# Optimization experiments

Hardware: AMD Instinct MI355X
Metric: run time of the kernel (lower is better)

## Reference

```python
import jax, jax.numpy as jnp
import numpy as np

DIM = 1024
HEADS = 16
HEAD_DIM = DIM // HEADS
NUM_PATCHES = 1024
B = 4
SCALE = float(HEAD_DIM) ** (-1)          # standparam=False
SCALE_ATTN_WEIGHTS = 1.0                  # softmax branch (use_relu=False)


def setup_inputs() -> dict:
    key = jax.random.key(0)
    k1, k2, k3, k4 = jax.random.split(key, 4)
    lim = 1.0 / np.sqrt(DIM)  # torch Linear default init range
    return {
        "hidden_states": jax.random.normal(k1, (B, NUM_PATCHES, DIM), dtype=jnp.float32),
        "attention_mask": jax.random.randint(k2, (B, NUM_PATCHES), 0, 2, dtype=jnp.int32),
        "Wq": jax.random.uniform(k3, (DIM, DIM), minval=-lim, maxval=lim, dtype=jnp.float32),
        "Wk": jax.random.uniform(k4, (DIM, DIM), minval=-lim, maxval=lim, dtype=jnp.float32),
        "gamma_1": jnp.float32(1.0),
        "gamma_2": jnp.float32(1.0),
        "gamma_3": jnp.float32(1.0),
    }


def reference(hidden_states, attention_mask, Wq, Wk, gamma_1, gamma_2, gamma_3):
    b, n, _ = hidden_states.shape
    # q, k projections (bias-free linear, torch convention: x @ W.T)
    q = hidden_states @ Wq.T  # [B, N, dim]
    k = hidden_states @ Wk.T
    q = q.reshape(b, n, HEADS, HEAD_DIM).transpose(0, 2, 1, 3)  # [B, H, N, D]
    k = k.reshape(b, n, HEADS, HEAD_DIM).transpose(0, 2, 1, 3)
    scores = jnp.einsum("bhnd,bhmd->bhnm", q, k) * SCALE  # [B, H, N, N]
    probs = SCALE_ATTN_WEIGHTS * jax.nn.softmax(scores, axis=-1)
    # shaped attention branch
    nonzero = (attention_mask == 0).astype(jnp.float32)  # [B, N]
    nnz = nonzero.sum(-1)[:, None, None]                 # [B, 1, 1]
    center = (nonzero[:, :, None] * nonzero[:, None, :]) / nnz  # [B, N, N]
    m = jnp.einsum("bn,nm->bnm", nonzero, jnp.eye(n, dtype=jnp.float32))  # diag_embed
    out = (gamma_1 * m[:, None, :, :]
           + gamma_2 * probs
           - gamma_3 * center[:, None, :, :])
    return out
```

## Files before the change

kernel.cpp:

```cpp
#include <hip/hip_runtime.h>
#include <hip/hip_bf16.h>

typedef __attribute__((ext_vector_type(8))) short short8;
typedef __attribute__((ext_vector_type(8))) unsigned short ushort8;
typedef __attribute__((ext_vector_type(4))) float floatx4;

#define B_SZ 4
#define N_SZ 1024
#define DIM_SZ 1024
#define H_SZ 16
#define HD_SZ 64
#define M_TOT 4096
#define QK_ELEMS (M_TOT * DIM_SZ)

__device__ __forceinline__ unsigned short f2bf(float x) {
  union { float f; unsigned u; } v; v.f = x;
  unsigned r = v.u + 0x7FFFu + ((v.u >> 16) & 1u);
  return (unsigned short)(r >> 16);
}

__global__ __launch_bounds__(256) void proj_qk(
    const float* __restrict__ hs,
    const float* __restrict__ Wq,
    const float* __restrict__ Wk,
    unsigned short* __restrict__ qk)
{
  const int which = blockIdx.z;
  const float* __restrict__ W = which ? Wk : Wq;
  unsigned short* __restrict__ outp = qk + (size_t)which * QK_ELEMS;

  const int tid = threadIdx.x;
  const int lane = tid & 63;
  const int wave = tid >> 6;
  const int mbase = blockIdx.x * 64;
  const int obase = blockIdx.y * 64;

  __shared__ unsigned short As[64][40];
  __shared__ unsigned short Bs[64][40];

  floatx4 zero = {0.f, 0.f, 0.f, 0.f};
  floatx4 acc00 = zero, acc01 = zero, acc10 = zero, acc11 = zero;

  const int lr = tid >> 2;
  const int lk = (tid & 3) * 8;
  const float* aptr = hs + (size_t)(mbase + lr) * DIM_SZ + lk;
  const float* bptr = W + (size_t)(obase + lr) * DIM_SZ + lk;

  const int fr = lane & 15;
  const int k8 = (lane >> 4) * 8;
  const int rb = (wave >> 1) * 32;
  const int cb = (wave & 1) * 32;

  for (int k0 = 0; k0 < DIM_SZ; k0 += 32) {
    floatx4 av0 = *reinterpret_cast<const floatx4*>(aptr + k0);
    floatx4 av1 = *reinterpret_cast<const floatx4*>(aptr + k0 + 4);
    floatx4 bv0 = *reinterpret_cast<const floatx4*>(bptr + k0);
    floatx4 bv1 = *reinterpret_cast<const floatx4*>(bptr + k0 + 4);
    ushort8 a8, b8;
#pragma unroll
    for (int j = 0; j < 4; ++j) {
      a8[j] = f2bf(av0[j]); a8[4 + j] = f2bf(av1[j]);
      b8[j] = f2bf(bv0[j]); b8[4 + j] = f2bf(bv1[j]);
    }
    *reinterpret_cast<ushort8*>(&As[lr][lk]) = a8;
    *reinterpret_cast<ushort8*>(&Bs[lr][lk]) = b8;
    __syncthreads();

    short8 a0 = *reinterpret_cast<const short8*>(&As[rb + fr][k8]);
    short8 a1 = *reinterpret_cast<const short8*>(&As[rb + 16 + fr][k8]);
    short8 b0 = *reinterpret_cast<const short8*>(&Bs[cb + fr][k8]);
    short8 b1 = *reinterpret_cast<const short8*>(&Bs[cb + 16 + fr][k8]);
    acc00 = __builtin_amdgcn_mfma_f32_16x16x32_bf16(a0, b0, acc00, 0, 0, 0);
    acc01 = __builtin_amdgcn_mfma_f32_16x16x32_bf16(a0, b1, acc01, 0, 0, 0);
    acc10 = __builtin_amdgcn_mfma_f32_16x16x32_bf16(a1, b0, acc10, 0, 0, 0);
    acc11 = __builtin_amdgcn_mfma_f32_16x16x32_bf16(a1, b1, acc11, 0, 0, 0);
    __syncthreads();
  }

  const int rrow = (lane >> 4) * 4;
#pragma unroll
  for (int mi = 0; mi < 2; ++mi) {
#pragma unroll
    for (int ni = 0; ni < 2; ++ni) {
      floatx4 a = (mi == 0) ? (ni == 0 ? acc00 : acc01) : (ni == 0 ? acc10 : acc11);
      int o = obase + cb + ni * 16 + fr;
      int h = o >> 6, d = o & 63;
#pragma unroll
      for (int r = 0; r < 4; ++r) {
        int mrow = mbase + rb + mi * 16 + rrow + r;
        int bb = mrow >> 10, n = mrow & 1023;
        outp[((size_t)((bb * H_SZ + h) * N_SZ + n)) * HD_SZ + d] = f2bf(a[r]);
      }
    }
  }
}

__global__ __launch_bounds__(256) void attn_out(
    const unsigned short* __restrict__ qk,
    const int* __restrict__ mask,
    const float* __restrict__ g1p,
    const float* __restrict__ g2p,
    const float* __restrict__ g3p,
    float* __restrict__ out)
{
  const int bh = blockIdx.y;
  const int b = bh >> 4;
  const int qbase = blockIdx.x * 16;
  const int tid = threadIdx.x;
  const int lane = tid & 63;
  const int wave = tid >> 6;

  __shared__ float nzf[N_SZ];
  __shared__ float wsum[4];
  __shared__ float rowsums[4][16];

  float cnt = 0.f;
  for (int i = tid; i < N_SZ; i += 256) {
    float v = (mask[b * N_SZ + i] == 0) ? 1.0f : 0.0f;
    nzf[i] = v;
    cnt += v;
  }
#pragma unroll
  for (int off = 32; off >= 1; off >>= 1) cnt += __shfl_xor(cnt, off);
  if (lane == 0) wsum[wave] = cnt;
  __syncthreads();
  const float nnz = wsum[0] + wsum[1] + wsum[2] + wsum[3];

  const int fr = lane & 15;
  const int k8 = (lane >> 4) * 8;

  const unsigned short* qptr =
      qk + ((size_t)(bh * N_SZ + qbase + fr)) * HD_SZ + k8;
  short8 qa0 = *reinterpret_cast<const short8*>(qptr);
  short8 qa1 = *reinterpret_cast<const short8*>(qptr + 32);

  const unsigned short* kbase = qk + (size_t)QK_ELEMS + (size_t)bh * N_SZ * HD_SZ;

  floatx4 zero = {0.f, 0.f, 0.f, 0.f};
  floatx4 acc[16];
#pragma unroll
  for (int c = 0; c < 16; ++c) acc[c] = zero;

#pragma unroll
  for (int c = 0; c < 16; ++c) {
    int col = wave * 256 + c * 16 + fr;
    const unsigned short* kp = kbase + (size_t)col * HD_SZ + k8;
    short8 kb0 = *reinterpret_cast<const short8*>(kp);
    short8 kb1 = *reinterpret_cast<const short8*>(kp + 32);
    acc[c] = __builtin_amdgcn_mfma_f32_16x16x32_bf16(qa0, kb0, acc[c], 0, 0, 0);
    acc[c] = __builtin_amdgcn_mfma_f32_16x16x32_bf16(qa1, kb1, acc[c], 0, 0, 0);
  }

  const float expscale = 0.015625f * 1.44269504f;
  float psum[4] = {0.f, 0.f, 0.f, 0.f};
#pragma unroll
  for (int c = 0; c < 16; ++c) {
#pragma unroll
    for (int r = 0; r < 4; ++r) {
      float p = __builtin_amdgcn_exp2f(acc[c][r] * expscale);
      acc[c][r] = p;
      psum[r] += p;
    }
  }
#pragma unroll
  for (int m = 1; m < 16; m <<= 1) {
#pragma unroll
    for (int r = 0; r < 4; ++r) psum[r] += __shfl_xor(psum[r], m);
  }
  if (fr == 0) {
#pragma unroll
    for (int r = 0; r < 4; ++r) rowsums[wave][(lane >> 4) * 4 + r] = psum[r];
  }
  __syncthreads();

  const float g1 = *g1p, g2 = *g2p, g3 = *g3p;
  const float g3n = g3 / nnz;
  float inv[4], nzq[4];
  int rowg[4];
#pragma unroll
  for (int r = 0; r < 4; ++r) {
    int rloc = (lane >> 4) * 4 + r;
    float rs = rowsums[0][rloc] + rowsums[1][rloc] + rowsums[2][rloc] + rowsums[3][rloc];
    inv[r] = g2 / rs;
    rowg[r] = qbase + rloc;
    nzq[r] = nzf[rowg[r]];
  }
#pragma unroll
  for (int c = 0; c < 16; ++c) {
    int col = wave * 256 + c * 16 + fr;
    float nzc = nzf[col];
#pragma unroll
    for (int r = 0; r < 4; ++r) {
      float v = acc[c][r] * inv[r] - g3n * nzq[r] * nzc;
      if (rowg[r] == col) v += g1 * nzq[r];
      out[((size_t)(bh * N_SZ + rowg[r])) * N_SZ + col] = v;
    }
  }
}

extern "C" void kernel_launch(void* const* d_in, const int* in_sizes, int n_in,
                              void* d_out, int out_size, void* d_ws, size_t ws_size,
                              hipStream_t stream) {
  const float* hs = (const float*)d_in[0];
  const int* mask = (const int*)d_in[1];
  const float* Wq = (const float*)d_in[2];
  const float* Wk = (const float*)d_in[3];
  const float* g1 = (const float*)d_in[4];
  const float* g2 = (const float*)d_in[5];
  const float* g3 = (const float*)d_in[6];
  float* out = (float*)d_out;
  unsigned short* qk = (unsigned short*)d_ws;

  proj_qk<<<dim3(M_TOT / 64, DIM_SZ / 64, 2), 256, 0, stream>>>(hs, Wq, Wk, qk);
  attn_out<<<dim3(N_SZ / 16, B_SZ * H_SZ), 256, 0, stream>>>(qk, mask, g1, g2, g3, out);
}
```

Baseline: 141.0 us.

## Pre-convert inputs to bf16 and use larger-tile fused QK projection GEMM

Adds a separate kernel that converts hidden states and both weight matrices to bf16 once. The projection becomes a single GEMM over the concatenated Wq/Wk outputs with 128x128 tiles, loading tiles straight into LDS via global_load_lds, and writes a row-major [M, 2048] Q|K buffer. The attention kernel now reads Q and K from that interleaved layout. This removes the repeated fp32-to-bf16 conversion inside the GEMM loop and increases MFMA reuse per LDS load, at the cost of an extra launch, extra workspace traffic, and strided K reads in the attention kernel.

```diff
diff --git a/kernel.cpp b/kernel.cpp
--- a/kernel.cpp
+++ b/kernel.cpp
@@ -11,7 +11,12 @@
 #define H_SZ 16
 #define HD_SZ 64
 #define M_TOT 4096
-#define QK_ELEMS (M_TOT * DIM_SZ)
+#define NOUT 2048
+#define HS_ELEMS 4194304
+#define W_ELEMS  1048576
+#define CVT_TOT  6291456
+#define WB_OFF   HS_ELEMS
+#define CB_OFF   CVT_TOT
 
 __device__ __forceinline__ unsigned short f2bf(float x) {
   union { float f; unsigned u; } v; v.f = x;
@@ -19,84 +24,87 @@
   return (unsigned short)(r >> 16);
 }
 
-__global__ __launch_bounds__(256) void proj_qk(
-    const float* __restrict__ hs,
-    const float* __restrict__ Wq,
-    const float* __restrict__ Wk,
-    unsigned short* __restrict__ qk)
+typedef const __attribute__((address_space(1))) void GASV;
+typedef __attribute__((address_space(3))) void LASV;
+#define GLL16(g, l) __builtin_amdgcn_global_load_lds((GASV*)(g), (LASV*)(l), 16, 0, 0)
+
+__global__ __launch_bounds__(256) void convert_bf16(
+    const float* __restrict__ hs, const float* __restrict__ Wq,
+    const float* __restrict__ Wk, unsigned short* __restrict__ ws)
 {
-  const int which = blockIdx.z;
-  const float* __restrict__ W = which ? Wk : Wq;
-  unsigned short* __restrict__ outp = qk + (size_t)which * QK_ELEMS;
-
-  const int tid = threadIdx.x;
-  const int lane = tid & 63;
-  const int wave = tid >> 6;
-  const int mbase = blockIdx.x * 64;
-  const int obase = blockIdx.y * 64;
-
-  __shared__ unsigned short As[64][40];
-  __shared__ unsigned short Bs[64][40];
-
-  floatx4 zero = {0.f, 0.f, 0.f, 0.f};
-  floatx4 acc00 = zero, acc01 = zero, acc10 = zero, acc11 = zero;
-
-  const int lr = tid >> 2;
-  const int lk = (tid & 3) * 8;
-  const float* aptr = hs + (size_t)(mbase + lr) * DIM_SZ + lk;
-  const float* bptr = W + (size_t)(obase + lr) * DIM_SZ + lk;
-
-  const int fr = lane & 15;
-  const int k8 = (lane >> 4) * 8;
-  const int rb = (wave >> 1) * 32;
-  const int cb = (wave & 1) * 32;
+  size_t i = ((size_t)blockIdx.x * 256 + threadIdx.x) * 8;
+  const float* src;
+  if (i < HS_ELEMS) src = hs + i;
+  else if (i < HS_ELEMS + W_ELEMS) src = Wq + (i - HS_ELEMS);
+  else src = Wk + (i - HS_ELEMS - W_ELEMS);
+  floatx4 v0 = *reinterpret_cast<const floatx4*>(src);
+  floatx4 v1 = *reinterpret_cast<const floatx4*>(src + 4);
+  ushort8 o;
+#pragma unroll
+  for (int j = 0; j < 4; ++j) { o[j] = f2bf(v0[j]); o[4 + j] = f2bf(v1[j]); }
+  *reinterpret_cast<ushort8*>(ws + i) = o;
+}
+
+__global__ __launch_bounds__(256) void proj_gemm(
+    const unsigned short* __restrict__ ws_ro, unsigned short* __restrict__ Cb)
+{
+  const unsigned short* hsb = ws_ro;
+  const unsigned short* Wb = ws_ro + WB_OFF;
+  __shared__ unsigned short As[128 * 32];
+  __shared__ unsigned short Bs[128 * 32];
+  const int tid = threadIdx.x, lane = tid & 63, wave = tid >> 6;
+  const int fr = lane & 15, k8 = (lane >> 4) * 8;
+  const int wr = wave >> 1, wc = wave & 1;
+  const int mbase = blockIdx.x * 128, obase = blockIdx.y * 128;
+
+  const unsigned short* ag = hsb + (size_t)(mbase + (tid >> 2)) * DIM_SZ + (tid & 3) * 8;
+  const unsigned short* bg = Wb + (size_t)(obase + (tid >> 2)) * DIM_SZ + (tid & 3) * 8;
+  unsigned short* lA = &As[tid * 8];
+  unsigned short* lB = &Bs[tid * 8];
+
+  floatx4 acc[4][4];
+#pragma unroll
+  for (int m = 0; m < 4; ++m)
+#pragma unroll
+    for (int n = 0; n < 4; ++n) acc[m][n] = floatx4{0.f, 0.f, 0.f, 0.f};
 
   for (int k0 = 0; k0 < DIM_SZ; k0 += 32) {
-    floatx4 av0 = *reinterpret_cast<const floatx4*>(aptr + k0);
-    floatx4 av1 = *reinterpret_cast<const floatx4*>(aptr + k0 + 4);
-    floatx4 bv0 = *reinterpret_cast<const floatx4*>(bptr + k0);
-    floatx4 bv1 = *reinterpret_cast<const floatx4*>(bptr + k0 + 4);
-    ushort8 a8, b8;
-#pragma unroll
-    for (int j = 0; j < 4; ++j) {
-      a8[j] = f2bf(av0[j]); a8[4 + j] = f2bf(av1[j]);
-      b8[j] = f2bf(bv0[j]); b8[4 + j] = f2bf(bv1[j]);
-    }
-    *reinterpret_cast<ushort8*>(&As[lr][lk]) = a8;
-    *reinterpret_cast<ushort8*>(&Bs[lr][lk]) = b8;
+    GLL16(ag + k0, lA);
+    GLL16(ag + k0 + 64 * DIM_SZ, lA + 2048);
+    GLL16(bg + k0, lB);
+    GLL16(bg + k0 + 64 * DIM_SZ, lB + 2048);
     __syncthreads();
-
-    short8 a0 = *reinterpret_cast<const short8*>(&As[rb + fr][k8]);
-    short8 a1 = *reinterpret_cast<const short8*>(&As[rb + 16 + fr][k8]);
-    short8 b0 = *reinterpret_cast<const short8*>(&Bs[cb + fr][k8]);
-    short8 b1 = *reinterpret_cast<const short8*>(&Bs[cb + 16 + fr][k8]);
-    acc00 = __builtin_amdgcn_mfma_f32_16x16x32_bf16(a0, b0, acc00, 0, 0, 0);
-    acc01 = __builtin_amdgcn_mfma_f32_16x16x32_bf16(a0, b1, acc01, 0, 0, 0);
-    acc10 = __builtin_amdgcn_mfma_f32_16x16x32_bf16(a1, b0, acc10, 0, 0, 0);
-    acc11 = __builtin_amdgcn_mfma_f32_16x16x32_bf16(a1, b1, acc11, 0, 0, 0);
+    short8 af[4], bfr[4];
+#pragma unroll
+    for (int m = 0; m < 4; ++m)
+      af[m] = *reinterpret_cast<const short8*>(&As[(wr * 64 + m * 16 + fr) * 32 + k8]);
+#pragma unroll
+    for (int n = 0; n < 4; ++n)
+      bfr[n] = *reinterpret_cast<const short8*>(&Bs[(wc * 64 + n * 16 + fr) * 32 + k8]);
+#pragma unroll
+    for (int m = 0; m < 4; ++m)
+#pragma unroll
+      for (int n = 0; n < 4; ++n)
+        acc[m][n] = __builtin_amdgcn_mfma_f32_16x16x32_bf16(af[m], bfr[n], acc[m][n], 0, 0, 0);
     __syncthreads();
   }
 
-  const int rrow = (lane >> 4) * 4;
-#pragma unroll
-  for (int mi = 0; mi < 2; ++mi) {
-#pragma unroll
-    for (int ni = 0; ni < 2; ++ni) {
-      floatx4 a = (mi == 0) ? (ni == 0 ? acc00 : acc01) : (ni == 0 ? acc10 : acc11);
-      int o = obase + cb + ni * 16 + fr;
-      int h = o >> 6, d = o & 63;
+  const int rr = (lane >> 4) * 4;
+#pragma unroll
+  for (int m = 0; m < 4; ++m)
+#pragma unroll
+    for (int n = 0; n < 4; ++n) {
+      int col = obase + wc * 64 + n * 16 + fr;
 #pragma unroll
       for (int r = 0; r < 4; ++r) {
-        int mrow = mbase + rb + mi * 16 + rrow + r;
-        int bb = mrow >> 10, n = mrow & 1023;
-        outp[((size_t)((bb * H_SZ + h) * N_SZ + n)) * HD_SZ + d] = f2bf(a[r]);
+        int row = mbase + wr * 64 + m * 16 + rr + r;
+        Cb[(size_t)row * NOUT + col] = f2bf(acc[m][n][r]);
       }
     }
-  }
 }
 
 __global__ __launch_bounds__(256) void attn_out(
-    const unsigned short* __restrict__ qk,
+    const unsigned short* __restrict__ Cb,
     const int* __restrict__ mask,
     const float* __restrict__ g1p,
     const float* __restrict__ g2p,
@@ -105,6 +113,7 @@
 {
   const int bh = blockIdx.y;
   const int b = bh >> 4;
+  const int h = bh & 15;
   const int qbase = blockIdx.x * 16;
   const int tid = threadIdx.x;
   const int lane = tid & 63;
@@ -130,21 +139,19 @@
   const int k8 = (lane >> 4) * 8;
 
   const unsigned short* qptr =
-      qk + ((size_t)(bh * N_SZ + qbase + fr)) * HD_SZ + k8;
+      Cb + (size_t)(b * N_SZ + qbase + fr) * NOUT + h * HD_SZ + k8;
   short8 qa0 = *reinterpret_cast<const short8*>(qptr);
   short8 qa1 = *reinterpret_cast<const short8*>(qptr + 32);
 
-  const unsigned short* kbase = qk + (size_t)QK_ELEMS + (size_t)bh * N_SZ * HD_SZ;
-
-  floatx4 zero = {0.f, 0.f, 0.f, 0.f};
   floatx4 acc[16];
 #pragma unroll
-  for (int c = 0; c < 16; ++c) acc[c] = zero;
+  for (int c = 0; c < 16; ++c) acc[c] = floatx4{0.f, 0.f, 0.f, 0.f};
 
 #pragma unroll
   for (int c = 0; c < 16; ++c) {
     int col = wave * 256 + c * 16 + fr;
-    const unsigned short* kp = kbase + (size_t)col * HD_SZ + k8;
+    const unsigned short* kp =
+        Cb + (size_t)(b * N_SZ + col) * NOUT + N_SZ + h * HD_SZ + k8;
     short8 kb0 = *reinterpret_cast<const short8*>(kp);
     short8 kb1 = *reinterpret_cast<const short8*>(kp + 32);
     acc[c] = __builtin_amdgcn_mfma_f32_16x16x32_bf16(qa0, kb0, acc[c], 0, 0, 0);
@@ -209,8 +216,10 @@
   const float* g2 = (const float*)d_in[5];
   const float* g3 = (const float*)d_in[6];
   float* out = (float*)d_out;
-  unsigned short* qk = (unsigned short*)d_ws;
-
-  proj_qk<<<dim3(M_TOT / 64, DIM_SZ / 64, 2), 256, 0, stream>>>(hs, Wq, Wk, qk);
-  attn_out<<<dim3(N_SZ / 16, B_SZ * H_SZ), 256, 0, stream>>>(qk, mask, g1, g2, g3, out);
-}
+  unsigned short* ws = (unsigned short*)d_ws;
+
+  convert_bf16<<<CVT_TOT / (256 * 8), 256, 0, stream>>>(hs, Wq, Wk, ws);
+  proj_gemm<<<dim3(M_TOT / 128, NOUT / 128), 256, 0, stream>>>(ws, ws + CB_OFF);
+  attn_out<<<dim3(N_SZ / 16, B_SZ * H_SZ), 256, 0, stream>>>(
+      ws + CB_OFF, mask, g1, g2, g3, out);
+}
```

Result: faster. 128.0 us (-9.2%).
